# Optimization experiments

Measured on AMD Instinct MI355X. Metric: run time of the kernel, lower is better.

The kernel has to match this reference:

```python
import jax, jax.numpy as jnp
import numpy as np

B, N, D, P_IN, P_OUT = 8, 2048, 32, 8, 4


def setup_inputs() -> dict:
    key = jax.random.key(0)
    k1, k2, k3, k4 = jax.random.split(key, 4)
    U = jax.random.normal(k1, (B, N, D, P_IN), dtype=jnp.float32)
    A = jax.random.uniform(k2, (B, N, N), dtype=jnp.float32)
    W_self = jax.random.normal(k3, (P_IN, P_OUT), dtype=jnp.float32) * 0.01
    W_neigh = jax.random.normal(k4, (P_IN, P_OUT), dtype=jnp.float32) * 0.01
    bias = jnp.zeros((1, 1, 1, P_OUT), dtype=jnp.float32)
    return {"U": U, "A": A, "W_self": W_self, "W_neigh": W_neigh, "bias": bias}


def _stiefel_projection(Y_flat):
    # Polar factor: Y = W S V^T  ->  proj = W V^T (same as Y @ (Y^T Y)^{-1/2})
    u, _, vt = jnp.linalg.svd(Y_flat, full_matrices=False)
    return u @ vt


def reference(U, A, W_self, W_neigh, bias):
    # U: (B,N,d,p_in); A: (B,N,N)
    M_self = jnp.einsum('bndi,io->bndo', U, W_self)
    M_neigh = jnp.einsum('bndi,io->bndo', U, W_neigh)
    # dense neighborhood aggregation: A @ reshape(M_neigh, (B,N,d*p_out))
    M_agg = jnp.einsum('bnm,bmdo->bndo', A, M_neigh)
    Y = jax.nn.relu(M_self + M_agg + bias)
    Y_flat = Y.reshape(B * N, D, P_OUT)
    U_proj = _stiefel_projection(Y_flat)
    return U_proj.reshape(B, N, D, P_OUT)
```

## Files before the change

### kernel.cpp

```cpp
#include <hip/hip_runtime.h>
#include <math.h>

constexpr int B_   = 8;
constexpr int N_   = 2048;
constexpr int D_   = 32;
constexpr int PIN  = 8;
constexpr int POUT = 4;
constexpr int COLS = 128;
constexpr int BM   = 32;
constexpr int BK   = 64;
constexpr int NT   = N_ / BK;

using f32x4  = __attribute__((ext_vector_type(4))) float;
using bf16x8 = __attribute__((ext_vector_type(8))) short;

__device__ __forceinline__ unsigned short f2bf(float f) {
    union { float f; unsigned u; } v; v.f = f;
    unsigned u = v.u + 0x7fffu + ((v.u >> 16) & 1u);
    return (unsigned short)(u >> 16);
}

__device__ __forceinline__ void dma16(const void* g, void* l) {
    __builtin_amdgcn_global_load_lds(
        (const __attribute__((address_space(1))) unsigned int*)g,
        (__attribute__((address_space(3))) unsigned int*)(uintptr_t)l,
        16, 0, 0);
}

__global__ __launch_bounds__(256) void mneigh_t_kernel(
    const float* __restrict__ U, const float* __restrict__ Wn,
    const float* __restrict__ Ws, unsigned short* __restrict__ Btg,
    float* __restrict__ Mself)
{
    const int bt = blockIdx.x;
    const int b  = bt >> 6;
    const int n0 = (bt & 63) * 32;
    const int t  = threadIdx.x;
    const int d  = t >> 3;
    const int ns = t & 7;

    float wn[PIN][POUT], ws[PIN][POUT];
#pragma unroll
    for (int p = 0; p < PIN; ++p)
#pragma unroll
        for (int o = 0; o < POUT; ++o) {
            wn[p][o] = Wn[p * POUT + o];
            ws[p][o] = Ws[p * POUT + o];
        }

    union { unsigned short s[4]; int2 v; } ob[POUT];
    const float* Ub = U + (((size_t)(b * N_ + n0 + ns * 4)) * D_ + d) * PIN;
#pragma unroll
    for (int ni = 0; ni < 4; ++ni) {
        const float4 u0 = *(const float4*)(Ub + (size_t)ni * D_ * PIN);
        const float4 u1 = *(const float4*)(Ub + (size_t)ni * D_ * PIN + 4);
        const float uu[8] = {u0.x, u0.y, u0.z, u0.w, u1.x, u1.y, u1.z, u1.w};
        float4 ms;
#pragma unroll
        for (int o = 0; o < POUT; ++o) {
            float sn = 0.f, ss = 0.f;
#pragma unroll
            for (int p = 0; p < PIN; ++p) {
                sn = fmaf(uu[p], wn[p][o], sn);
                ss = fmaf(uu[p], ws[p][o], ss);
            }
            ob[o].s[ni] = f2bf(sn);
            ((float*)&ms)[o] = ss;
        }
        *(float4*)(Mself + ((size_t)(b * N_ + n0 + ns * 4 + ni)) * COLS + d * 4) = ms;
    }
#pragma unroll
    for (int o = 0; o < POUT; ++o) {
        unsigned short* dst =
            Btg + ((size_t)(b * COLS + d * 4 + o)) * N_ + n0 + ns * 4;
        *(int2*)dst = ob[o].v;
    }
}

__global__ __launch_bounds__(512) void gemm_proj_kernel(
    const float* __restrict__ A, const unsigned short* __restrict__ Btg,
    const float* __restrict__ Mself, const float* __restrict__ bias,
    float* __restrict__ out)
{
    __shared__ unsigned char smem[49152];
    float* Yl = (float*)smem;
    float* Gp = (float*)(smem + 16896);
    float* Sm = (float*)(smem + 22016);

    const int bid = (blockIdx.x & 7) * 64 + (blockIdx.x >> 3);
    const int b   = bid >> 6;
    const int r0  = (bid & 63) * BM;
    const int t   = threadIdx.x;
    const int lane = t & 63, wv = t >> 6;
    const int wr = wv >> 2, wc = wv & 3;
    const int q = lane >> 4, rl = lane & 15;
    const unsigned swzA = (unsigned)((lane & 7) << 5);
    const unsigned swzB = (unsigned)((lane & 7) << 4);
    const int rA = wr * 16 + rl;

    const char* Ab = (const char*)(A + (size_t)b * N_ * N_ + (size_t)r0 * N_);
    const char* Bb = (const char*)(Btg + (size_t)b * COLS * N_);

    const int arow = t >> 4;
    const unsigned ainner =
        ((unsigned)((t & 15) * 16)) ^ ((unsigned)((arow & 7) << 5));
    const char* a_src = Ab + (size_t)arow * (N_ * 4) + ainner;
    const int bcol = t >> 3;
    const unsigned binner =
        ((unsigned)((t & 7) * 16)) ^ ((unsigned)((bcol & 7) << 4));
    const char* b_src0 = Bb + (size_t)bcol * (N_ * 2) + binner;
    const char* b_src1 = Bb + (size_t)(bcol + 64) * (N_ * 2) + binner;

    unsigned char* a_dst = smem + wv * 1024;
    unsigned char* b_dst = smem + 16384 + wv * 1024;

#define STAGE(K0, BUF)                                                   \
    do {                                                                 \
        dma16(a_src + (size_t)(K0) * 4, a_dst + (BUF) * 8192);           \
        dma16(b_src0 + (size_t)(K0) * 2, b_dst + (BUF) * 16384);         \
        dma16(b_src1 + (size_t)(K0) * 2, b_dst + (BUF) * 16384 + 8192);  \
    } while (0)

    f32x4 acc[2] = {f32x4{0, 0, 0, 0}, f32x4{0, 0, 0, 0}};

    STAGE(0, 0);
    STAGE(BK, 1);
    asm volatile("s_waitcnt vmcnt(3)" ::: "memory");
    __builtin_amdgcn_s_barrier();

    for (int kt = 0; kt < NT; ++kt) {
        const unsigned cur = (unsigned)(kt & 1);
        const unsigned abase = cur * 8192u;
        const unsigned bbase = 16384u + cur * 16384u;
        __builtin_amdgcn_s_setprio(1);
#pragma unroll
        for (int ks = 0; ks < 2; ++ks) {
            const unsigned aoff = ((unsigned)(ks * 128 + q * 32)) ^ swzA;
            const float4 alo =
                *(const float4*)(smem + abase + rA * 256 + aoff);
            const float4 ahi =
                *(const float4*)(smem + abase + rA * 256 + aoff + 16);
            union { unsigned u[4]; bf16x8 v; } af;
            asm("v_cvt_pk_bf16_f32 %0, %1, %2"
                : "=v"(af.u[0]) : "v"(alo.x), "v"(alo.y));
            asm("v_cvt_pk_bf16_f32 %0, %1, %2"
                : "=v"(af.u[1]) : "v"(alo.z), "v"(alo.w));
            asm("v_cvt_pk_bf16_f32 %0, %1, %2"
                : "=v"(af.u[2]) : "v"(ahi.x), "v"(ahi.y));
            asm("v_cvt_pk_bf16_f32 %0, %1, %2"
                : "=v"(af.u[3]) : "v"(ahi.z), "v"(ahi.w));
#pragma unroll
            for (int cf = 0; cf < 2; ++cf) {
                const int rB = wc * 32 + cf * 16 + rl;
                const bf16x8 bfr = *(const bf16x8*)(
                    smem + bbase + rB * 128 +
                    (((unsigned)(ks * 64 + q * 16)) ^ swzB));
                acc[cf] = __builtin_amdgcn_mfma_f32_16x16x32_bf16(
                    af.v, bfr, acc[cf], 0, 0, 0);
            }
        }
        __builtin_amdgcn_s_setprio(0);
        __builtin_amdgcn_s_barrier();
        const int k2 = (kt + 2 < NT) ? (kt + 2) * BK : 0;
        STAGE(k2, cur);
        asm volatile("s_waitcnt vmcnt(3)" ::: "memory");
        __builtin_amdgcn_s_barrier();
    }
#undef STAGE
    __syncthreads();

#pragma unroll
    for (int cf = 0; cf < 2; ++cf)
#pragma unroll
        for (int r = 0; r < 4; ++r) {
            const int row = wr * 16 + q * 4 + r;
            const int col = wc * 32 + cf * 16 + rl;
            Yl[row * 132 + col] = acc[cf][r];
        }
    __syncthreads();

    const float bz[4] = {bias[0], bias[1], bias[2], bias[3]};
    const float* Mb = Mself + ((size_t)(b * N_ + r0)) * COLS;
#pragma unroll
    for (int i = 0; i < 2; ++i) {
        const int cell = t + i * 512;
        const int row = cell >> 5, d = cell & 31;
        const float4 m = *(const float4*)(Mb + (size_t)row * COLS + d * 4);
        const int idx = row * 132 + d * 4;
        float4 y = *(const float4*)(Yl + idx);
        y.x = fmaxf(y.x + m.x + bz[0], 0.f);
        y.y = fmaxf(y.y + m.y + bz[1], 0.f);
        y.z = fmaxf(y.z + m.z + bz[2], 0.f);
        y.w = fmaxf(y.w + m.w + bz[3], 0.f);
        *(float4*)(Yl + idx) = y;
    }
    __syncthreads();

    if (t < 128) {
        const int row = t >> 2, qd = t & 3;
        float g[10] = {0,0,0,0,0,0,0,0,0,0};
#pragma unroll
        for (int d = qd * 8; d < qd * 8 + 8; ++d) {
            const float4 y = *(const float4*)(Yl + row * 132 + 4 * d);
            g[0] = fmaf(y.x, y.x, g[0]); g[1] = fmaf(y.x, y.y, g[1]);
            g[2] = fmaf(y.x, y.z, g[2]); g[3] = fmaf(y.x, y.w, g[3]);
            g[4] = fmaf(y.y, y.y, g[4]); g[5] = fmaf(y.y, y.z, g[5]);
            g[6] = fmaf(y.y, y.w, g[6]); g[7] = fmaf(y.z, y.z, g[7]);
            g[8] = fmaf(y.z, y.w, g[8]); g[9] = fmaf(y.w, y.w, g[9]);
        }
        float* gp = Gp + (row * 4 + qd) * 10;
#pragma unroll
        for (int k = 0; k < 10; ++k) gp[k] = g[k];
    }
    __syncthreads();

    if (t < 32) {
        float gg[10];
#pragma unroll
        for (int k = 0; k < 10; ++k)
            gg[k] = Gp[(t * 4 + 0) * 10 + k] + Gp[(t * 4 + 1) * 10 + k] +
                    Gp[(t * 4 + 2) * 10 + k] + Gp[(t * 4 + 3) * 10 + k];
        float m[4][4] = {{gg[0], gg[1], gg[2], gg[3]},
                         {gg[1], gg[4], gg[5], gg[6]},
                         {gg[2], gg[5], gg[7], gg[8]},
                         {gg[3], gg[6], gg[8], gg[9]}};
        float v[4][4] = {{1,0,0,0},{0,1,0,0},{0,0,1,0},{0,0,0,1}};
        for (int sweep = 0; sweep < 6; ++sweep) {
#pragma unroll
            for (int p = 0; p < 3; ++p) {
#pragma unroll
                for (int qq = p + 1; qq < 4; ++qq) {
                    const float apq = m[p][qq];
                    if (fabsf(apq) < 1e-28f) continue;
                    const float theta = (m[qq][qq] - m[p][p]) / (2.f * apq);
                    const float tt = copysignf(1.f, theta) /
                        (fabsf(theta) + sqrtf(fmaf(theta, theta, 1.f)));
                    const float c = 1.f / sqrtf(fmaf(tt, tt, 1.f));
                    const float s = tt * c;
#pragma unroll
                    for (int k = 0; k < 4; ++k) {
                        const float mkp = m[k][p], mkq = m[k][qq];
                        m[k][p] = c * mkp - s * mkq;
                        m[k][qq] = s * mkp + c * mkq;
                    }
#pragma unroll
                    for (int k = 0; k < 4; ++k) {
                        const float mpk = m[p][k], mqk = m[qq][k];
                        m[p][k] = c * mpk - s * mqk;
                        m[qq][k] = s * mpk + c * mqk;
                    }
#pragma unroll
                    for (int k = 0; k < 4; ++k) {
                        const float vkp = v[k][p], vkq = v[k][qq];
                        v[k][p] = c * vkp - s * vkq;
                        v[k][qq] = s * vkp + c * vkq;
                    }
                }
            }
        }
        const float lam[4] = {m[0][0], m[1][1], m[2][2], m[3][3]};
        const float lmax = fmaxf(fmaxf(lam[0], lam[1]), fmaxf(lam[2], lam[3]));
        const float lfloor = fmaxf(lmax * 1e-12f, 1e-30f);
        float rlv[4];
#pragma unroll
        for (int k = 0; k < 4; ++k) rlv[k] = 1.f / sqrtf(fmaxf(lam[k], lfloor));
#pragma unroll
        for (int i = 0; i < 4; ++i)
#pragma unroll
            for (int j = 0; j < 4; ++j)
                Sm[t * 16 + i * 4 + j] =
                    v[i][0] * v[j][0] * rlv[0] + v[i][1] * v[j][1] * rlv[1] +
                    v[i][2] * v[j][2] * rlv[2] + v[i][3] * v[j][3] * rlv[3];
    }
    __syncthreads();

#pragma unroll
    for (int i = 0; i < 2; ++i) {
        const int cell = t + i * 512;
        const int row = cell >> 5, d = cell & 31;
        const float4 y = *(const float4*)(Yl + row * 132 + 4 * d);
        const float* S = Sm + row * 16;
        float4 o4;
        o4.x = y.x * S[0]  + y.y * S[4]  + y.z * S[8]  + y.w * S[12];
        o4.y = y.x * S[1]  + y.y * S[5]  + y.z * S[9]  + y.w * S[13];
        o4.z = y.x * S[2]  + y.y * S[6]  + y.z * S[10] + y.w * S[14];
        o4.w = y.x * S[3]  + y.y * S[7]  + y.z * S[11] + y.w * S[15];
        *(float4*)(out + ((size_t)(b * N_ + r0 + row)) * COLS + 4 * d) = o4;
    }
}

extern "C" void kernel_launch(void* const* d_in, const int* in_sizes, int n_in,
                              void* d_out, int out_size, void* d_ws, size_t ws_size,
                              hipStream_t stream)
{
    const float* U      = (const float*)d_in[0];
    const float* A      = (const float*)d_in[1];
    const float* Wself  = (const float*)d_in[2];
    const float* Wneigh = (const float*)d_in[3];
    const float* bias   = (const float*)d_in[4];
    float* out = (float*)d_out;

    unsigned short* Btg = (unsigned short*)d_ws;
    float* Mself = (float*)((char*)d_ws + (size_t)B_ * COLS * N_ * 2);

    mneigh_t_kernel<<<B_ * (N_ / 32), 256, 0, stream>>>(U, Wneigh, Wself, Btg,
                                                        Mself);
    gemm_proj_kernel<<<B_ * (N_ / BM), 512, 0, stream>>>(A, Btg, Mself, bias,
                                                         out);
}
```

Baseline: 50.08 us.

## Split GEMM over K halves with larger row tiles and separate reduce-projection kernel

The fused GEMM+projection kernel is split into a split-K GEMM, where each block handles 64 rows and half of K and writes fp32 partials, and a new reduce kernel. The reduce kernel sums the two partials, adds Mself and bias, applies relu and computes the polar projection. The larger row tile halves B-matrix reloads per row and the K split keeps the grid at 512 blocks. The cost is an extra kernel launch and a round trip of partial sums through global memory (about 16 MB written and read).

New measurement: 52.30 us. 4.4% more time.

```diff
diff --git a/kernel.cpp b/kernel.cpp
--- a/kernel.cpp
+++ b/kernel.cpp
@@ -7,9 +7,10 @@
 constexpr int PIN  = 8;
 constexpr int POUT = 4;
 constexpr int COLS = 128;
-constexpr int BM   = 32;
+constexpr int BM   = 64;
 constexpr int BK   = 64;
-constexpr int NT   = N_ / BK;
+constexpr int KH   = 1024;
+constexpr int NT2  = KH / BK;
 
 using f32x4  = __attribute__((ext_vector_type(4))) float;
 using bf16x8 = __attribute__((ext_vector_type(8))) short;
@@ -77,69 +78,74 @@
     }
 }
 
-__global__ __launch_bounds__(512) void gemm_proj_kernel(
+__global__ __launch_bounds__(512) void gemm_part_kernel(
     const float* __restrict__ A, const unsigned short* __restrict__ Btg,
-    const float* __restrict__ Mself, const float* __restrict__ bias,
-    float* __restrict__ out)
+    float* __restrict__ Cp)
 {
-    __shared__ unsigned char smem[49152];
-    float* Yl = (float*)smem;
-    float* Gp = (float*)(smem + 16896);
-    float* Sm = (float*)(smem + 22016);
-
-    const int bid = (blockIdx.x & 7) * 64 + (blockIdx.x >> 3);
-    const int b   = bid >> 6;
-    const int r0  = (bid & 63) * BM;
+    __shared__ unsigned char smem[65536];
+
+    const int sid = (blockIdx.x & 7) * 64 + (blockIdx.x >> 3);
+    const int b   = sid >> 6;
+    const int rem = sid & 63;
+    const int r0  = (rem >> 1) * BM;
+    const int kh  = rem & 1;
     const int t   = threadIdx.x;
     const int lane = t & 63, wv = t >> 6;
-    const int wr = wv >> 2, wc = wv & 3;
+    const int wr = wv >> 1, wc = wv & 1;
     const int q = lane >> 4, rl = lane & 15;
-    const unsigned swzA = (unsigned)((lane & 7) << 5);
-    const unsigned swzB = (unsigned)((lane & 7) << 4);
     const int rA = wr * 16 + rl;
-
-    const char* Ab = (const char*)(A + (size_t)b * N_ * N_ + (size_t)r0 * N_);
-    const char* Bb = (const char*)(Btg + (size_t)b * COLS * N_);
-
-    const int arow = t >> 4;
-    const unsigned ainner =
-        ((unsigned)((t & 15) * 16)) ^ ((unsigned)((arow & 7) << 5));
-    const char* a_src = Ab + (size_t)arow * (N_ * 4) + ainner;
+    const unsigned aswzr = (unsigned)((rA & 15) << 4);
+
+    const char* Ab = (const char*)(A + (size_t)b * N_ * N_ + (size_t)r0 * N_ +
+                                   (size_t)kh * KH);
+    const char* Bb = (const char*)(Btg + (size_t)b * COLS * N_ + (size_t)kh * KH);
+
+    const int ar0 = wv * 8 + (lane >> 4);
+    const int ar1 = ar0 + 4;
+    const unsigned ain0 =
+        ((unsigned)((lane & 15) * 16)) ^ ((unsigned)((ar0 & 15) << 4));
+    const unsigned ain1 =
+        ((unsigned)((lane & 15) * 16)) ^ ((unsigned)((ar1 & 15) << 4));
+    const char* a_src0 = Ab + (size_t)ar0 * (N_ * 4) + ain0;
+    const char* a_src1 = Ab + (size_t)ar1 * (N_ * 4) + ain1;
+    unsigned char* a_dst0 = smem + wv * 2048;
+    unsigned char* a_dst1 = smem + wv * 2048 + 1024;
+
     const int bcol = t >> 3;
     const unsigned binner =
         ((unsigned)((t & 7) * 16)) ^ ((unsigned)((bcol & 7) << 4));
     const char* b_src0 = Bb + (size_t)bcol * (N_ * 2) + binner;
     const char* b_src1 = Bb + (size_t)(bcol + 64) * (N_ * 2) + binner;
-
-    unsigned char* a_dst = smem + wv * 1024;
-    unsigned char* b_dst = smem + 16384 + wv * 1024;
-
-#define STAGE(K0, BUF)                                                   \
-    do {                                                                 \
-        dma16(a_src + (size_t)(K0) * 4, a_dst + (BUF) * 8192);           \
-        dma16(b_src0 + (size_t)(K0) * 2, b_dst + (BUF) * 16384);         \
-        dma16(b_src1 + (size_t)(K0) * 2, b_dst + (BUF) * 16384 + 8192);  \
+    unsigned char* b_dst0 = smem + 32768 + wv * 1024;
+    unsigned char* b_dst1 = smem + 32768 + 8192 + wv * 1024;
+
+#define STAGE(KB, BUF)                                           \
+    do {                                                         \
+        dma16(a_src0 + (size_t)(KB) * 4, a_dst0 + (BUF) * 16384);\
+        dma16(a_src1 + (size_t)(KB) * 4, a_dst1 + (BUF) * 16384);\
+        dma16(b_src0 + (size_t)(KB) * 2, b_dst0 + (BUF) * 16384);\
+        dma16(b_src1 + (size_t)(KB) * 2, b_dst1 + (BUF) * 16384);\
     } while (0)
 
-    f32x4 acc[2] = {f32x4{0, 0, 0, 0}, f32x4{0, 0, 0, 0}};
+    f32x4 acc[4] = {f32x4{0,0,0,0}, f32x4{0,0,0,0},
+                    f32x4{0,0,0,0}, f32x4{0,0,0,0}};
 
     STAGE(0, 0);
     STAGE(BK, 1);
-    asm volatile("s_waitcnt vmcnt(3)" ::: "memory");
+    asm volatile("s_waitcnt vmcnt(4)" ::: "memory");
     __builtin_amdgcn_s_barrier();
 
-    for (int kt = 0; kt < NT; ++kt) {
+    for (int kt = 0; kt < NT2; ++kt) {
         const unsigned cur = (unsigned)(kt & 1);
-        const unsigned abase = cur * 8192u;
-        const unsigned bbase = 16384u + cur * 16384u;
+        const unsigned abase = cur * 16384u;
+        const unsigned bbase = 32768u + cur * 16384u;
         __builtin_amdgcn_s_setprio(1);
 #pragma unroll
         for (int ks = 0; ks < 2; ++ks) {
-            const unsigned aoff = ((unsigned)(ks * 128 + q * 32)) ^ swzA;
-            const float4 alo =
-                *(const float4*)(smem + abase + rA * 256 + aoff);
-            const float4 ahi =
-                *(const float4*)(smem + abase + rA * 256 + aoff + 16);
+            const unsigned off0 = ((unsigned)(ks * 128 + q * 32)) ^ aswzr;
+            const unsigned off1 = ((unsigned)(ks * 128 + q * 32 + 16)) ^ aswzr;
+            const float4 alo = *(const float4*)(smem + abase + rA * 256 + off0);
+            const float4 ahi = *(const float4*)(smem + abase + rA * 256 + off1);
             union { unsigned u[4]; bf16x8 v; } af;
             asm("v_cvt_pk_bf16_f32 %0, %1, %2"
                 : "=v"(af.u[0]) : "v"(alo.x), "v"(alo.y));
@@ -150,49 +156,65 @@
             asm("v_cvt_pk_bf16_f32 %0, %1, %2"
                 : "=v"(af.u[3]) : "v"(ahi.z), "v"(ahi.w));
 #pragma unroll
-            for (int cf = 0; cf < 2; ++cf) {
-                const int rB = wc * 32 + cf * 16 + rl;
+            for (int cf = 0; cf < 4; ++cf) {
+                const int rB = wc * 64 + cf * 16 + rl;
                 const bf16x8 bfr = *(const bf16x8*)(
                     smem + bbase + rB * 128 +
-                    (((unsigned)(ks * 64 + q * 16)) ^ swzB));
+                    (((unsigned)(ks * 64 + q * 16)) ^ ((unsigned)((rB & 7) << 4))));
                 acc[cf] = __builtin_amdgcn_mfma_f32_16x16x32_bf16(
                     af.v, bfr, acc[cf], 0, 0, 0);
             }
         }
         __builtin_amdgcn_s_setprio(0);
         __builtin_amdgcn_s_barrier();
-        const int k2 = (kt + 2 < NT) ? (kt + 2) * BK : 0;
-        STAGE(k2, cur);
-        asm volatile("s_waitcnt vmcnt(3)" ::: "memory");
+        const int kb2 = (kt + 2 < NT2) ? (kt + 2) * BK : 0;
+        STAGE(kb2, cur);
+        asm volatile("s_waitcnt vmcnt(4)" ::: "memory");
         __builtin_amdgcn_s_barrier();
     }
 #undef STAGE
-    __syncthreads();
-
-#pragma unroll
-    for (int cf = 0; cf < 2; ++cf)
-#pragma unroll
-        for (int r = 0; r < 4; ++r) {
-            const int row = wr * 16 + q * 4 + r;
-            const int col = wc * 32 + cf * 16 + rl;
-            Yl[row * 132 + col] = acc[cf][r];
-        }
-    __syncthreads();
-
+    asm volatile("s_waitcnt vmcnt(0)" ::: "memory");
+
+    float* Cb = Cp + (((size_t)(kh * 8 + b)) * N_ + r0) * COLS;
+#pragma unroll
+    for (int cf = 0; cf < 4; ++cf)
+#pragma unroll
+        for (int r = 0; r < 4; ++r)
+            Cb[(size_t)(wr * 16 + q * 4 + r) * COLS + wc * 64 + cf * 16 + rl] =
+                acc[cf][r];
+}
+
+__global__ __launch_bounds__(256) void reduce_proj_kernel(
+    const float* __restrict__ Cp, const float* __restrict__ Mself,
+    const float* __restrict__ bias, float* __restrict__ out)
+{
+    __shared__ unsigned char smemr[24064];
+    float* Yl = (float*)smemr;
+    float* Gp = (float*)(smemr + 16896);
+    float* Sm = (float*)(smemr + 22016);
+
+    const int bid = blockIdx.x;
+    const int b   = bid >> 6;
+    const int r0  = (bid & 63) * 32;
+    const int t   = threadIdx.x;
     const float bz[4] = {bias[0], bias[1], bias[2], bias[3]};
-    const float* Mb = Mself + ((size_t)(b * N_ + r0)) * COLS;
-#pragma unroll
-    for (int i = 0; i < 2; ++i) {
-        const int cell = t + i * 512;
+    const size_t base = ((size_t)(b * N_ + r0)) * COLS;
+    const size_t halfoff = (size_t)8 * N_ * COLS;
+
+#pragma unroll
+    for (int i = 0; i < 4; ++i) {
+        const int cell = t + i * 256;
         const int row = cell >> 5, d = cell & 31;
-        const float4 m = *(const float4*)(Mb + (size_t)row * COLS + d * 4);
-        const int idx = row * 132 + d * 4;
-        float4 y = *(const float4*)(Yl + idx);
-        y.x = fmaxf(y.x + m.x + bz[0], 0.f);
-        y.y = fmaxf(y.y + m.y + bz[1], 0.f);
-        y.z = fmaxf(y.z + m.z + bz[2], 0.f);
-        y.w = fmaxf(y.w + m.w + bz[3], 0.f);
-        *(float4*)(Yl + idx) = y;
+        const size_t idx = base + (size_t)row * COLS + d * 4;
+        const float4 p0 = *(const float4*)(Cp + idx);
+        const float4 p1 = *(const float4*)(Cp + idx + halfoff);
+        const float4 m  = *(const float4*)(Mself + idx);
+        float4 y;
+        y.x = fmaxf(p0.x + p1.x + m.x + bz[0], 0.f);
+        y.y = fmaxf(p0.y + p1.y + m.y + bz[1], 0.f);
+        y.z = fmaxf(p0.z + p1.z + m.z + bz[2], 0.f);
+        y.w = fmaxf(p0.w + p1.w + m.w + bz[3], 0.f);
+        *(float4*)(Yl + row * 132 + d * 4) = y;
     }
     __syncthreads();
 
@@ -275,8 +297,8 @@
     __syncthreads();
 
 #pragma unroll
-    for (int i = 0; i < 2; ++i) {
-        const int cell = t + i * 512;
+    for (int i = 0; i < 4; ++i) {
+        const int cell = t + i * 256;
         const int row = cell >> 5, d = cell & 31;
         const float4 y = *(const float4*)(Yl + row * 132 + 4 * d);
         const float* S = Sm + row * 16;
@@ -285,7 +307,7 @@
         o4.y = y.x * S[1]  + y.y * S[5]  + y.z * S[9]  + y.w * S[13];
         o4.z = y.x * S[2]  + y.y * S[6]  + y.z * S[10] + y.w * S[14];
         o4.w = y.x * S[3]  + y.y * S[7]  + y.z * S[11] + y.w * S[15];
-        *(float4*)(out + ((size_t)(b * N_ + r0 + row)) * COLS + 4 * d) = o4;
+        *(float4*)(out + base + (size_t)row * COLS + 4 * d) = o4;
     }
 }
 
@@ -301,10 +323,11 @@
     float* out = (float*)d_out;
 
     unsigned short* Btg = (unsigned short*)d_ws;
-    float* Mself = (float*)((char*)d_ws + (size_t)B_ * COLS * N_ * 2);
-
-    mneigh_t_kernel<<<B_ * (N_ / 32), 256, 0, stream>>>(U, Wneigh, Wself, Btg,
-                                                        Mself);
-    gemm_proj_kernel<<<B_ * (N_ / BM), 512, 0, stream>>>(A, Btg, Mself, bias,
-                                                         out);
-}
+    float* Mself = (float*)((char*)d_ws + (size_t)4 * 1024 * 1024);
+    float* Cp    = (float*)((char*)d_ws + (size_t)12  * 1024 * 1024 +
+                            (size_t)512 * 1024);
+
+    mneigh_t_kernel<<<512, 256, 0, stream>>>(U, Wneigh, Wself, Btg, Mself);
+    gemm_part_kernel<<<512, 512, 0, stream>>>(A, Btg, Cp);
+    reduce_proj_kernel<<<512, 256, 0, stream>>>(Cp, Mself, bias, out);
+}
```

## Double GEMM row tile and switch to triple-buffered async LDS pipeline

Applied to the files above, without the earlier changes.

Doubles the row tile from 32 to 64, which halves the grid to 256 blocks and lets each block reuse every B tile for twice as many A rows. Each wave now computes four 16-column MFMA fragments instead of two. The two-stage LDS double buffer with two barriers per iteration becomes a three-stage ring, with vmcnt waits issued before the single top barrier, to hide more load latency. In exchange it uses 96KB of LDS and launch bounds of one block per CU, so occupancy and parallelism drop: only 256 blocks run across the CUs.

Result: slower. 56.69 us (+13.2%).

```diff
diff --git a/kernel.cpp b/kernel.cpp
--- a/kernel.cpp
+++ b/kernel.cpp
@@ -7,7 +7,7 @@
 constexpr int PIN  = 8;
 constexpr int POUT = 4;
 constexpr int COLS = 128;
-constexpr int BM   = 32;
+constexpr int BM   = 64;
 constexpr int BK   = 64;
 constexpr int NT   = N_ / BK;
 
@@ -77,69 +77,73 @@
     }
 }
 
-__global__ __launch_bounds__(512) void gemm_proj_kernel(
+__global__ __launch_bounds__(512, 1) void gemm_proj_kernel(
     const float* __restrict__ A, const unsigned short* __restrict__ Btg,
     const float* __restrict__ Mself, const float* __restrict__ bias,
     float* __restrict__ out)
 {
-    __shared__ unsigned char smem[49152];
+    __shared__ unsigned char smem[98304];
     float* Yl = (float*)smem;
-    float* Gp = (float*)(smem + 16896);
-    float* Sm = (float*)(smem + 22016);
-
-    const int bid = (blockIdx.x & 7) * 64 + (blockIdx.x >> 3);
-    const int b   = bid >> 6;
-    const int r0  = (bid & 63) * BM;
+    float* Gp = (float*)(smem + 33792);
+    float* Sm = (float*)(smem + 44032);
+
+    const int bid = (blockIdx.x & 7) * 32 + (blockIdx.x >> 3);
+    const int b   = bid >> 5;
+    const int r0  = (bid & 31) * BM;
     const int t   = threadIdx.x;
     const int lane = t & 63, wv = t >> 6;
-    const int wr = wv >> 2, wc = wv & 3;
+    const int wr = wv >> 1, wc = wv & 1;
     const int q = lane >> 4, rl = lane & 15;
-    const unsigned swzA = (unsigned)((lane & 7) << 5);
-    const unsigned swzB = (unsigned)((lane & 7) << 4);
     const int rA = wr * 16 + rl;
+    const unsigned arx = (unsigned)((rA & 15) << 4);
 
     const char* Ab = (const char*)(A + (size_t)b * N_ * N_ + (size_t)r0 * N_);
     const char* Bb = (const char*)(Btg + (size_t)b * COLS * N_);
 
-    const int arow = t >> 4;
-    const unsigned ainner =
-        ((unsigned)((t & 15) * 16)) ^ ((unsigned)((arow & 7) << 5));
-    const char* a_src = Ab + (size_t)arow * (N_ * 4) + ainner;
-    const int bcol = t >> 3;
-    const unsigned binner =
-        ((unsigned)((t & 7) * 16)) ^ ((unsigned)((bcol & 7) << 4));
-    const char* b_src0 = Bb + (size_t)bcol * (N_ * 2) + binner;
-    const char* b_src1 = Bb + (size_t)(bcol + 64) * (N_ * 2) + binner;
-
-    unsigned char* a_dst = smem + wv * 1024;
-    unsigned char* b_dst = smem + 16384 + wv * 1024;
-
-#define STAGE(K0, BUF)                                                   \
-    do {                                                                 \
-        dma16(a_src + (size_t)(K0) * 4, a_dst + (BUF) * 8192);           \
-        dma16(b_src0 + (size_t)(K0) * 2, b_dst + (BUF) * 16384);         \
-        dma16(b_src1 + (size_t)(K0) * 2, b_dst + (BUF) * 16384 + 8192);  \
+    const int arow = wv * 4 + (lane >> 4);
+    const unsigned ain = ((unsigned)((lane & 15) * 16)) ^
+                         ((unsigned)((arow & 15) << 4));
+    const char* a_src0 = Ab + (size_t)arow * 8192 + ain;
+    const char* a_src1 = a_src0 + (size_t)32 * 8192;
+    const int bcol = wv * 8 + (lane >> 3);
+    const unsigned bin = ((unsigned)((lane & 7) * 16)) ^
+                         ((unsigned)((bcol & 7) << 4));
+    const char* b_src0 = Bb + (size_t)bcol * 4096 + bin;
+    const char* b_src1 = b_src0 + (size_t)64 * 4096;
+
+#define STAGE(K0, BUF)                                                \
+    do {                                                              \
+        unsigned char* ad = smem + (BUF) * 16384 + wv * 1024;         \
+        unsigned char* bd = smem + 49152 + (BUF) * 16384 + wv * 1024; \
+        dma16(a_src0 + (size_t)(K0) * 4, ad);                         \
+        dma16(a_src1 + (size_t)(K0) * 4, ad + 8192);                  \
+        dma16(b_src0 + (size_t)(K0) * 2, bd);                         \
+        dma16(b_src1 + (size_t)(K0) * 2, bd + 8192);                  \
     } while (0)
 
-    f32x4 acc[2] = {f32x4{0, 0, 0, 0}, f32x4{0, 0, 0, 0}};
+    f32x4 acc[4] = {f32x4{0,0,0,0}, f32x4{0,0,0,0},
+                    f32x4{0,0,0,0}, f32x4{0,0,0,0}};
 
     STAGE(0, 0);
     STAGE(BK, 1);
-    asm volatile("s_waitcnt vmcnt(3)" ::: "memory");
-    __builtin_amdgcn_s_barrier();
-
+    STAGE(2 * BK, 2);
+
+    int bufsel = 0;
     for (int kt = 0; kt < NT; ++kt) {
-        const unsigned cur = (unsigned)(kt & 1);
-        const unsigned abase = cur * 8192u;
-        const unsigned bbase = 16384u + cur * 16384u;
+        if (kt < NT - 2)       asm volatile("s_waitcnt vmcnt(8)" ::: "memory");
+        else if (kt == NT - 2) asm volatile("s_waitcnt vmcnt(4)" ::: "memory");
+        else                   asm volatile("s_waitcnt vmcnt(0)" ::: "memory");
+        __builtin_amdgcn_s_barrier();
+
+        const unsigned abase = (unsigned)bufsel * 16384u;
+        const unsigned bbase = 49152u + (unsigned)bufsel * 16384u;
         __builtin_amdgcn_s_setprio(1);
 #pragma unroll
         for (int ks = 0; ks < 2; ++ks) {
-            const unsigned aoff = ((unsigned)(ks * 128 + q * 32)) ^ swzA;
-            const float4 alo =
-                *(const float4*)(smem + abase + rA * 256 + aoff);
-            const float4 ahi =
-                *(const float4*)(smem + abase + rA * 256 + aoff + 16);
+            const unsigned off0 = ((unsigned)(ks * 128 + q * 32)) ^ arx;
+            const unsigned off1 = ((unsigned)(ks * 128 + q * 32 + 16)) ^ arx;
+            const float4 alo = *(const float4*)(smem + abase + rA * 256 + off0);
+            const float4 ahi = *(const float4*)(smem + abase + rA * 256 + off1);
             union { unsigned u[4]; bf16x8 v; } af;
             asm("v_cvt_pk_bf16_f32 %0, %1, %2"
                 : "=v"(af.u[0]) : "v"(alo.x), "v"(alo.y));
@@ -150,31 +154,30 @@
             asm("v_cvt_pk_bf16_f32 %0, %1, %2"
                 : "=v"(af.u[3]) : "v"(ahi.z), "v"(ahi.w));
 #pragma unroll
-            for (int cf = 0; cf < 2; ++cf) {
-                const int rB = wc * 32 + cf * 16 + rl;
+            for (int cf = 0; cf < 4; ++cf) {
+                const int rB = wc * 64 + cf * 16 + rl;
                 const bf16x8 bfr = *(const bf16x8*)(
                     smem + bbase + rB * 128 +
-                    (((unsigned)(ks * 64 + q * 16)) ^ swzB));
+                    (((unsigned)(ks * 64 + q * 16)) ^ ((unsigned)((rB & 7) << 4))));
                 acc[cf] = __builtin_amdgcn_mfma_f32_16x16x32_bf16(
                     af.v, bfr, acc[cf], 0, 0, 0);
             }
         }
         __builtin_amdgcn_s_setprio(0);
         __builtin_amdgcn_s_barrier();
-        const int k2 = (kt + 2 < NT) ? (kt + 2) * BK : 0;
-        STAGE(k2, cur);
-        asm volatile("s_waitcnt vmcnt(3)" ::: "memory");
-        __builtin_amdgcn_s_barrier();
+        if (kt + 3 < NT) STAGE((kt + 3) * BK, bufsel);
+        bufsel = (bufsel == 2) ? 0 : bufsel + 1;
     }
 #undef STAGE
-    __syncthreads();
-
-#pragma unroll
-    for (int cf = 0; cf < 2; ++cf)
+    asm volatile("s_waitcnt vmcnt(0)" ::: "memory");
+    __syncthreads();
+
+#pragma unroll
+    for (int cf = 0; cf < 4; ++cf)
 #pragma unroll
         for (int r = 0; r < 4; ++r) {
             const int row = wr * 16 + q * 4 + r;
-            const int col = wc * 32 + cf * 16 + rl;
+            const int col = wc * 64 + cf * 16 + rl;
             Yl[row * 132 + col] = acc[cf][r];
         }
     __syncthreads();
@@ -182,7 +185,7 @@
     const float bz[4] = {bias[0], bias[1], bias[2], bias[3]};
     const float* Mb = Mself + ((size_t)(b * N_ + r0)) * COLS;
 #pragma unroll
-    for (int i = 0; i < 2; ++i) {
+    for (int i = 0; i < 4; ++i) {
         const int cell = t + i * 512;
         const int row = cell >> 5, d = cell & 31;
         const float4 m = *(const float4*)(Mb + (size_t)row * COLS + d * 4);
@@ -196,7 +199,7 @@
     }
     __syncthreads();
 
-    if (t < 128) {
+    if (t < 256) {
         const int row = t >> 2, qd = t & 3;
         float g[10] = {0,0,0,0,0,0,0,0,0,0};
 #pragma unroll
@@ -214,7 +217,7 @@
     }
     __syncthreads();
 
-    if (t < 32) {
+    if (t < 64) {
         float gg[10];
 #pragma unroll
         for (int k = 0; k < 10; ++k)
@@ -275,7 +278,7 @@
     __syncthreads();
 
 #pragma unroll
-    for (int i = 0; i < 2; ++i) {
+    for (int i = 0; i < 4; ++i) {
         const int cell = t + i * 512;
         const int row = cell >> 5, d = cell & 31;
         const float4 y = *(const float4*)(Yl + row * 132 + 4 * d);
@@ -301,10 +304,8 @@
     float* out = (float*)d_out;
 
     unsigned short* Btg = (unsigned short*)d_ws;
-    float* Mself = (float*)((char*)d_ws + (size_t)B_ * COLS * N_ * 2);
-
-    mneigh_t_kernel<<<B_ * (N_ / 32), 256, 0, stream>>>(U, Wneigh, Wself, Btg,
-                                                        Mself);
-    gemm_proj_kernel<<<B_ * (N_ / BM), 512, 0, stream>>>(A, Btg, Mself, bias,
-                                                         out);
-}
+    float* Mself = (float*)((char*)d_ws + (size_t)4 * 1024 * 1024);
+
+    mneigh_t_kernel<<<512, 256, 0, stream>>>(U, Wneigh, Wself, Btg, Mself);
+    gemm_proj_kernel<<<256, 512, 0, stream>>>(A, Btg, Mself, bias, out);
+}
```
